# Kernel tuning notes

Hardware: AMD Instinct MI355X
Metric: run time of the kernel (lower is better)

Reference implementation:

```python
import jax, jax.numpy as jnp
import numpy as np

V = 32            # number_variables
K = 16            # degree + 1 spline coefficients per pair
DEG = 3           # cubic B-spline order for basis evaluation
LO, HI = -5.0, 5.0
SPAN_FACTOR = 0.1
N_SAMPLES = 131072
P_PAIRS = V * (V - 1) // 2  # 496


def bspline_basis(x):
    """Cubic B-spline basis with K clamped-uniform basis functions on the
    span_factor-expanded range [LO - s, HI + s].  x: [N] -> [N, K]."""
    s = SPAN_FACTOR * (HI - LO)
    lo, hi = LO - s, HI + s
    n_break = K - DEG + 1
    inner = jnp.linspace(lo, hi, n_break)
    t = jnp.concatenate([jnp.full((DEG,), lo), inner, jnp.full((DEG,), hi)])  # [K+DEG+1]
    x = jnp.clip(x, lo, hi - 1e-6 * (hi - lo))
    xb = x[:, None]
    # order-0 indicator functions: [N, K+DEG]
    B = ((xb >= t[None, :-1]) & (xb < t[None, 1:])).astype(x.dtype)
    for r in range(1, DEG + 1):
        tl, tr = t[:-(r + 1)], t[r:-1]
        den1 = tr - tl
        left = jnp.where(den1 > 0, (xb - tl) / jnp.where(den1 > 0, den1, 1.0), 0.0)
        tl2, tr2 = t[1:-r], t[r + 1:]
        den2 = tr2 - tl2
        right = jnp.where(den2 > 0, (tr2 - xb) / jnp.where(den2 > 0, den2, 1.0), 0.0)
        B = left * B[:, :-1] + right * B[:, 1:]
    return B  # [N, K]


def setup_inputs() -> dict:
    key = jax.random.key(0)
    k1, k2 = jax.random.split(key)
    inp = jax.random.normal(k1, (N_SAMPLES, V), dtype=jnp.float32)
    # learned spline coefficients, one column per (var, covar) pair,
    # initialized near the module's 0.1 constant init
    params = 0.1 + 0.05 * jax.random.normal(k2, (K, P_PAIRS), dtype=jnp.float32)
    return {"input": inp, "params": params}


def reference(input, params):
    # output[:, v] = input[:, v] + sum_{c < v} lambda_{v,c}(input[:, c]) * input[:, c]
    # In forward (non-inverse) mode every lambda depends only on `input`, so all
    # V*(V-1)/2 pairs are computed in one batched contraction instead of a loop.
    Basis = jax.vmap(bspline_basis)(input.T)  # [V, N, K], basis per covariate column
    idx_v, idx_c = np.tril_indices(V, -1)      # pair order matches params_index = v*(v-1)/2 + c
    P_mat = jnp.zeros((V, K, V), dtype=input.dtype).at[idx_c, :, idx_v].set(params.T)
    contrib = jnp.einsum('cnk,ckv->cnv', Basis, P_mat)   # lambda_{v,c}(x_{n,c})
    out = input + jnp.einsum('cnv,nc->nv', contrib, input)
    return out
```

## Files before the change

kernel.cpp:

```cpp
#include <hip/hip_runtime.h>
#include <hip/hip_bf16.h>


#define PPAIR 496

typedef _Float16 f16x8 __attribute__((ext_vector_type(8)));
typedef float f32x4 __attribute__((ext_vector_type(4)));
typedef unsigned int u32;
typedef unsigned int u32x4 __attribute__((ext_vector_type(4)));

__global__ __launch_bounds__(256) void prep_w2t(const float* __restrict__ params,
                                                unsigned short* __restrict__ w2t) {
    int idx = blockIdx.x * 256 + threadIdx.x;
    int v = idx >> 9;
    int c = (idx >> 4) & 31, k = idx & 15;
    float w = 0.0f;
    if (c < v) w = params[k * PPAIR + (v * (v - 1)) / 2 + c];
    _Float16 h = (_Float16)w;
    w2t[idx] = __builtin_bit_cast(unsigned short, h);
}

__global__ __launch_bounds__(256, 3) void decor_main(const float* __restrict__ xin,
                                                     const unsigned short* __restrict__ w2t,
                                                     float* __restrict__ out) {
    const int tid = threadIdx.x;
    const int wv = tid >> 6;
    const int l = tid & 63;
    const int s = l & 15;
    const int q = l >> 4;
    const int qp = q & 1;
    const int sigma = ((q & 1) << 1) | (q >> 1);

    f16x8 b1[8][2];
    f16x8 b0[4][2];
#pragma unroll
    for (int u = 0; u < 8; ++u) {
#pragma unroll
        for (int e = 0; e < 2; ++e) {
            int t = 2 * u + (qp ? (1 - e) : e);
            b1[u][e] = *(const f16x8*)(w2t + (16 + s) * 512 + t * 32 + q * 8);
            if (u < 4) b0[u][e] = *(const f16x8*)(w2t + s * 512 + t * 32 + q * 8);
        }
    }

    const float sc = 13.0f / 12.0f;
    const int S0w = blockIdx.x * 256 + wv * 64;

    float xv[8];
    {
        const float* xr = xin + (S0w + s) * 32 + sigma;
#pragma unroll
        for (int u = 0; u < 8; ++u) xv[u] = xr[4 * u];
    }

#pragma unroll
    for (int tile = 0; tile < 4; ++tile) {
        const int T0 = S0w + tile * 16;

        float xe0[4], xe1[4];
#pragma unroll
        for (int rI = 0; rI < 4; ++rI) {
            int base = (T0 + q * 4 + rI) * 32;
            xe0[rI] = xin[base + s];
            xe1[rI] = xin[base + 16 + s];
        }
        float xvn[8];
        if (tile < 3) {
            const float* xr = xin + (T0 + 16 + s) * 32 + sigma;
#pragma unroll
            for (int u = 0; u < 8; ++u) xvn[u] = xr[4 * u];
        }

        f32x4 acc0 = {0.f, 0.f, 0.f, 0.f};
        f32x4 acc1 = {0.f, 0.f, 0.f, 0.f};

#pragma unroll
        for (int u = 0; u < 8; ++u) {
            float x = xv[u];
            float uu = fmaf(x, sc, 6.5f);
            uu = fminf(fmaxf(uu, 0.0f), 12.999987f);
            int mi = (int)uu;
            float mf = (float)mi;
            float r = uu - mf;
            float N0, N1, N2, N3;
            if (__all(mi >= 3 && mi <= 9)) {
                float omr = 1.0f - r;
                float r2 = r * r, r3 = r2 * r;
                float o2 = omr * omr;
                N0 = o2 * omr * (1.0f / 6.0f);
                N3 = r3 * (1.0f / 6.0f);
                N1 = fmaf(0.5f, r3, (2.0f / 3.0f) - r2);
                N2 = 1.0f - N0 - N1 - N3;
            } else {
                float t13 = 13.0f - mf;
                float af = fminf(mf, 1.0f);
                float bf = fminf(mf, 2.0f);
                float cf = fminf(t13, 2.0f);
                float df = fminf(t13, 3.0f);
                float r1 = 1.0f - r;
                float l2 = r + af, rr2 = cf - r;
                float l3 = r + bf, rr3 = df - r;
                float iv = (af == 0.0f) ? 1.0f : 0.5f;
                float T = r1 * iv;
                float M0 = r1 * T;
                float sv = l2 * T;
                float iv2 = (cf == 1.0f) ? 1.0f : 0.5f;
                float T2 = r * iv2;
                float M1 = fmaf(rr2, T2, sv);
                float M2 = r * T2;
                float iv3 = 0.5f;
                iv3 = (bf == 0.0f) ? 1.0f : iv3;
                iv3 = (bf == 2.0f) ? (1.0f / 3.0f) : iv3;
                T = M0 * iv3;
                N0 = r1 * T;
                sv = l3 * T;
                float g14 = af + cf;
                float iv4 = (g14 == 2.0f) ? 0.5f : (1.0f / 3.0f);
                T = M1 * iv4;
                N1 = fmaf(rr2, T, sv);
                sv = l2 * T;
                float iv5 = 0.5f;
                iv5 = (df == 1.0f) ? 1.0f : iv5;
                iv5 = (df == 3.0f) ? (1.0f / 3.0f) : iv5;
                T = M2 * iv5;
                N2 = fmaf(rr3, T, sv);
                N3 = r * T;
            }
            float g0 = x * N0, g1 = x * N1, g2 = x * N2, g3 = x * N3;
            int e = mi & 1;
            float aa = e ? 0.0f : g0, bb = e ? g0 : g1;
            float cc = e ? g1 : g2, dd = e ? g2 : g3;
            float ee = e ? g3 : 0.0f;
            u32 p0 = __builtin_bit_cast(u32, __builtin_amdgcn_cvt_pkrtz(aa, bb));
            u32 p1 = __builtin_bit_cast(u32, __builtin_amdgcn_cvt_pkrtz(cc, dd));
            u32 p2 = __builtin_bit_cast(u32, __builtin_amdgcn_cvt_pkrtz(ee, 0.0f));
            int w0 = mi >> 1;
            int dlt = w0 & 1;
            u32 C0 = dlt ? 0u : p0;
            u32 C1 = dlt ? p0 : p1;
            u32 C2 = dlt ? p1 : p2;
            u32 C3 = dlt ? p2 : 0u;
            int j0 = (w0 & 6) ^ (qp << 2);
            bool b2 = (j0 & 2) != 0;
            u32 t0 = b2 ? 0u : C0;
            u32 t1 = b2 ? 0u : C1;
            u32 t2 = b2 ? C0 : C2;
            u32 t3 = b2 ? C1 : C3;
            u32 t4 = b2 ? C2 : 0u;
            u32 t5 = b2 ? C3 : 0u;
            bool b4 = (j0 & 4) != 0;
            u32 B0 = b4 ? t4 : t0;
            u32 B1 = b4 ? t5 : t1;
            u32 B2 = b4 ? 0u : t2;
            u32 B3 = b4 ? 0u : t3;
            u32 B4 = b4 ? t0 : t4;
            u32 B5 = b4 ? t1 : t5;
            u32 B6 = b4 ? t2 : 0u;
            u32 B7 = b4 ? t3 : 0u;
            u32 R0 = (u32)__shfl_xor((int)B4, 16);
            u32 R1 = (u32)__shfl_xor((int)B5, 16);
            u32 R2 = (u32)__shfl_xor((int)B6, 16);
            u32 R3 = (u32)__shfl_xor((int)B7, 16);
            u32x4 kp = {B0, B1, B2, B3};
            u32x4 rc = {R0, R1, R2, R3};
            f16x8 ka = __builtin_bit_cast(f16x8, kp);
            f16x8 ra = __builtin_bit_cast(f16x8, rc);
            acc1 = __builtin_amdgcn_mfma_f32_16x16x32_f16(ka, b1[u][0], acc1, 0, 0, 0);
            acc1 = __builtin_amdgcn_mfma_f32_16x16x32_f16(ra, b1[u][1], acc1, 0, 0, 0);
            if (u < 4) {
                acc0 = __builtin_amdgcn_mfma_f32_16x16x32_f16(ka, b0[u][0], acc0, 0, 0, 0);
                acc0 = __builtin_amdgcn_mfma_f32_16x16x32_f16(ra, b0[u][1], acc0, 0, 0, 0);
            }
        }

#pragma unroll
        for (int rI = 0; rI < 4; ++rI) {
            int sample = T0 + q * 4 + rI;
            int base = sample * 32;
            out[base + s]      = xe0[rI] + acc0[rI];
            out[base + 16 + s] = xe1[rI] + acc1[rI];
        }

        if (tile < 3) {
#pragma unroll
            for (int u = 0; u < 8; ++u) xv[u] = xvn[u];
        }
    }
}

extern "C" void kernel_launch(void* const* d_in, const int* in_sizes, int n_in,
                              void* d_out, int out_size, void* d_ws, size_t ws_size,
                              hipStream_t stream) {
    const float* xin = (const float*)d_in[0];
    const float* params = (const float*)d_in[1];
    float* out = (float*)d_out;
    unsigned short* w2t = (unsigned short*)d_ws;

    prep_w2t<<<64, 256, 0, stream>>>(params, w2t);
    decor_main<<<512, 256, 0, stream>>>(xin, w2t, out);
}
```

Baseline: 84.62 us.

## Drop cross-lane shuffles by having each lane evaluate basis for its own covariates

Changes the work split so each lane evaluates spline bases for 16 covariate values directly, instead of 8 values plus shuffles to swap halves between lanes. The weight staging layout is changed to match, and the four shfl_xor per step are removed. This doubles the per-lane basis evaluation ALU work and register use (xv grows to 16), and lowers the occupancy hint from 3 to 2 blocks. The intent is to cut cross-lane permute latency at the cost of redundant math.

```diff
diff --git a/kernel.cpp b/kernel.cpp
--- a/kernel.cpp
+++ b/kernel.cpp
@@ -11,16 +11,17 @@
 
 __global__ __launch_bounds__(256) void prep_w2t(const float* __restrict__ params,
                                                 unsigned short* __restrict__ w2t) {
-    int idx = blockIdx.x * 256 + threadIdx.x;
-    int v = idx >> 9;
-    int c = (idx >> 4) & 31, k = idx & 15;
+    int i = blockIdx.x * 256 + threadIdx.x;
+    int c = i & 31;
+    int k = (i >> 5) & 15;
+    int v = i >> 9;
     float w = 0.0f;
     if (c < v) w = params[k * PPAIR + (v * (v - 1)) / 2 + c];
     _Float16 h = (_Float16)w;
-    w2t[idx] = __builtin_bit_cast(unsigned short, h);
+    w2t[v * 512 + c * 16 + k] = __builtin_bit_cast(unsigned short, h);
 }
 
-__global__ __launch_bounds__(256, 3) void decor_main(const float* __restrict__ xin,
+__global__ __launch_bounds__(256, 2) void decor_main(const float* __restrict__ xin,
                                                      const unsigned short* __restrict__ w2t,
                                                      float* __restrict__ out) {
     const int tid = threadIdx.x;
@@ -29,28 +30,24 @@
     const int s = l & 15;
     const int q = l >> 4;
     const int qp = q & 1;
-    const int sigma = ((q & 1) << 1) | (q >> 1);
+    const int qh = q >> 1;
 
-    f16x8 b1[8][2];
-    f16x8 b0[4][2];
+    f16x8 b1[16];
+    f16x8 b0[8];
 #pragma unroll
-    for (int u = 0; u < 8; ++u) {
-#pragma unroll
-        for (int e = 0; e < 2; ++e) {
-            int t = 2 * u + (qp ? (1 - e) : e);
-            b1[u][e] = *(const f16x8*)(w2t + (16 + s) * 512 + t * 32 + q * 8);
-            if (u < 4) b0[u][e] = *(const f16x8*)(w2t + s * 512 + t * 32 + q * 8);
-        }
+    for (int t = 0; t < 16; ++t) {
+        b1[t] = *(const f16x8*)(w2t + (16 + s) * 512 + t * 32 + q * 8);
+        if (t < 8) b0[t] = *(const f16x8*)(w2t + s * 512 + t * 32 + q * 8);
     }
 
     const float sc = 13.0f / 12.0f;
     const int S0w = blockIdx.x * 256 + wv * 64;
 
-    float xv[8];
+    float xv[16];
     {
-        const float* xr = xin + (S0w + s) * 32 + sigma;
+        const float* xr = xin + (S0w + s) * 32 + qh;
 #pragma unroll
-        for (int u = 0; u < 8; ++u) xv[u] = xr[4 * u];
+        for (int t = 0; t < 16; ++t) xv[t] = xr[2 * t];
     }
 
 #pragma unroll
@@ -64,19 +61,19 @@
             xe0[rI] = xin[base + s];
             xe1[rI] = xin[base + 16 + s];
         }
-        float xvn[8];
+        float xvn[16];
         if (tile < 3) {
-            const float* xr = xin + (T0 + 16 + s) * 32 + sigma;
+            const float* xr = xin + (T0 + 16 + s) * 32 + qh;
 #pragma unroll
-            for (int u = 0; u < 8; ++u) xvn[u] = xr[4 * u];
+            for (int t = 0; t < 16; ++t) xvn[t] = xr[2 * t];
         }
 
         f32x4 acc0 = {0.f, 0.f, 0.f, 0.f};
         f32x4 acc1 = {0.f, 0.f, 0.f, 0.f};
 
 #pragma unroll
-        for (int u = 0; u < 8; ++u) {
-            float x = xv[u];
+        for (int t = 0; t < 16; ++t) {
+            float x = xv[t];
             float uu = fmaf(x, sc, 6.5f);
             uu = fminf(fmaxf(uu, 0.0f), 12.999987f);
             int mi = (int)uu;
@@ -153,23 +150,11 @@
             u32 B1 = b4 ? t5 : t1;
             u32 B2 = b4 ? 0u : t2;
             u32 B3 = b4 ? 0u : t3;
-            u32 B4 = b4 ? t0 : t4;
-            u32 B5 = b4 ? t1 : t5;
-            u32 B6 = b4 ? t2 : 0u;
-            u32 B7 = b4 ? t3 : 0u;
-            u32 R0 = (u32)__shfl_xor((int)B4, 16);
-            u32 R1 = (u32)__shfl_xor((int)B5, 16);
-            u32 R2 = (u32)__shfl_xor((int)B6, 16);
-            u32 R3 = (u32)__shfl_xor((int)B7, 16);
             u32x4 kp = {B0, B1, B2, B3};
-            u32x4 rc = {R0, R1, R2, R3};
             f16x8 ka = __builtin_bit_cast(f16x8, kp);
-            f16x8 ra = __builtin_bit_cast(f16x8, rc);
-            acc1 = __builtin_amdgcn_mfma_f32_16x16x32_f16(ka, b1[u][0], acc1, 0, 0, 0);
-            acc1 = __builtin_amdgcn_mfma_f32_16x16x32_f16(ra, b1[u][1], acc1, 0, 0, 0);
-            if (u < 4) {
-                acc0 = __builtin_amdgcn_mfma_f32_16x16x32_f16(ka, b0[u][0], acc0, 0, 0, 0);
-                acc0 = __builtin_amdgcn_mfma_f32_16x16x32_f16(ra, b0[u][1], acc0, 0, 0, 0);
+            acc1 = __builtin_amdgcn_mfma_f32_16x16x32_f16(ka, b1[t], acc1, 0, 0, 0);
+            if (t < 8) {
+                acc0 = __builtin_amdgcn_mfma_f32_16x16x32_f16(ka, b0[t], acc0, 0, 0, 0);
             }
         }
 
@@ -183,7 +168,7 @@
 
         if (tile < 3) {
 #pragma unroll
-            for (int u = 0; u < 8; ++u) xv[u] = xvn[u];
+            for (int t = 0; t < 16; ++t) xv[t] = xvn[t];
         }
     }
 }
```

New measurement: 93.13 us. 1.1x slower.
